# Performance work log

Measured on AMD Instinct MI355X. Metric: run time of the kernel, lower is better.

Reference implementation:

```python
import jax, jax.numpy as jnp
import numpy as np

KERNEL = 3  # unfold kernel size (stride 1, no padding)

def _unfold(x, k):
    # torch.nn.Unfold(kernel_size=k) equivalent: (B, C, H, W) -> (B, C*k*k, L)
    # channel ordering: index = c*k*k + i*k + j (channel outermost), matching torch.
    B, C, H, W = x.shape
    Ho, Wo = H - k + 1, W - k + 1
    cols = [x[:, :, i:i + Ho, j:j + Wo] for i in range(k) for j in range(k)]  # k*k x (B,C,Ho,Wo)
    u = jnp.stack(cols, axis=2)  # (B, C, k*k, Ho, Wo)
    return u.reshape(B, C * k * k, Ho * Wo)


def setup_inputs() -> dict:
    key = jax.random.key(0)
    k1, k2, k3, k4 = jax.random.split(key, 4)
    B, C, H, W = 512, 3, 64, 64
    M = 512            # num_neurons
    K = C * KERNEL * KERNEL   # input_dim = 27
    L = (H - KERNEL + 1) * (W - KERNEL + 1)  # 3844 patches
    O = 10             # output_dim
    x = jax.random.normal(k1, (B, C, H, W), dtype=jnp.float32)
    G = jax.random.normal(k2, (M, L), dtype=jnp.float32)
    # original inits v,w to zeros; use randn for a non-degenerate reference
    v = jax.random.normal(k3, (M, K, O), dtype=jnp.float32) * 0.02
    w = jax.random.normal(k4, (M, K, O), dtype=jnp.float32) * 0.02
    return {"x": x, "G": G, "v": v, "w": w}


def reference(x, G, v, w):
    # Faithful to:
    #   U = unfold(x)                         (B, K, L)
    #   t = einsum('mn,ikn->imnk', G, U)      (B, M, L, K)  <- never materialized here
    #   out = einsum('ijkl,jlm->im', t, v-w)  (B, O)
    # Reordered as two small contractions (same math, no huge intermediate):
    U = _unfold(x, KERNEL)                    # (B, K, L)
    A = jnp.einsum('bkn,mn->bmk', U, G)       # (B, M, K): contract over patches L
    p_diff = v - w                            # (M, K, O)
    out = jnp.einsum('bmk,mko->bo', A, p_diff)  # (B, O)
    return out
```

## Files before the change

### kernel.cpp

```cpp
#include <hip/hip_runtime.h>
#include <hip/hip_bf16.h>

#define ODIM   10
#define HOg    62
#define LDIM   3844
#define CHW    12288
#define BATCH  512
#define KO     270
#define KOP2   288
#define MDIM   512
#define NPAD   3968
#define LROW   72

typedef __attribute__((ext_vector_type(8))) short bfrag;
typedef __attribute__((ext_vector_type(4))) float f32x4;

__global__ __launch_bounds__(256)
void prep_kernel(const float* __restrict__ G,
                 const float* __restrict__ v, const float* __restrict__ w,
                 __hip_bfloat16* __restrict__ Gt,
                 __hip_bfloat16* __restrict__ Pdt,
                 float* __restrict__ out) {
    const int b = blockIdx.x;
    if (b < 496) {
        __shared__ float tile[64][65];
        const int nTile = b % 62;
        const int mTile = b / 62;
        const int n0 = nTile * 64;
        const int m0 = mTile * 64;
        const int tc = threadIdx.x & 63;
        const int tr = threadIdx.x >> 6;
#pragma unroll
        for (int rr = 0; rr < 64; rr += 4) {
            int n = n0 + tc;
            tile[rr + tr][tc] = (n < LDIM) ? G[(size_t)(m0 + rr + tr) * LDIM + n] : 0.f;
        }
        __syncthreads();
        const int nr = threadIdx.x >> 2;
        const int ms = (threadIdx.x & 3) * 16;
        __hip_bfloat16 buf[16];
#pragma unroll
        for (int i = 0; i < 16; ++i)
            buf[i] = __float2bfloat16(tile[ms + i][nr]);
        __hip_bfloat16* dst = Gt + (size_t)(n0 + nr) * MDIM + m0 + ms;
        *reinterpret_cast<uint4*>(dst)     = *reinterpret_cast<uint4*>(&buf[0]);
        *reinterpret_cast<uint4*>(dst + 8) = *reinterpret_cast<uint4*>(&buf[8]);
    } else if (b < 1072) {
        int idx = (b - 496) * 256 + threadIdx.x;
        int ko = idx >> 9;
        int m  = idx & 511;
        float val = (ko < KO) ? (v[m * KO + ko] - w[m * KO + ko]) : 0.f;
        Pdt[idx] = __float2bfloat16(val);
    } else {
        int idx = (b - 1072) * 256 + threadIdx.x;
        out[idx] = 0.f;
    }
}

__global__ __launch_bounds__(256, 2)
void tmfma_kernel(const __hip_bfloat16* __restrict__ Pdt,
                  const __hip_bfloat16* __restrict__ Gt,
                  float* __restrict__ T) {
    const int orig = blockIdx.x;
    const int xcd  = orig & 7;
    const int q8   = orig >> 3;
    const int lb   = (xcd < 7 ? xcd * 35 : 245) + (xcd < 7 ? q8 : q8);
    const int lbf  = (xcd < 7 ? xcd * 35 + q8 : 245 + q8);
    const int kt   = lbf % 9;
    const int nt   = lbf / 9;
    (void)lb;
    const int ko0  = kt * 32;
    const int n0   = nt * 128;

    const int tid  = threadIdx.x;
    const int wv   = tid >> 6;
    const int lane = tid & 63;
    const int r16  = lane & 15;
    const int kg   = lane >> 4;

    __shared__ __hip_bfloat16 ldsA[2][32 * LROW];
    __shared__ __hip_bfloat16 ldsB[2][128 * LROW];

    const int srow  = tid >> 3;
    const int slot  = tid & 7;
    const __hip_bfloat16* pA = Pdt + (size_t)(ko0 + srow) * MDIM + slot * 8;
    const __hip_bfloat16* pB0 = Gt + (size_t)(n0 +       srow) * MDIM + slot * 8;
    const __hip_bfloat16* pB1 = Gt + (size_t)(n0 +  32 + srow) * MDIM + slot * 8;
    const __hip_bfloat16* pB2 = Gt + (size_t)(n0 +  64 + srow) * MDIM + slot * 8;
    const __hip_bfloat16* pB3 = Gt + (size_t)(n0 +  96 + srow) * MDIM + slot * 8;
    const int aoff  = srow * LROW + slot * 8;
    const int boff0 = (      srow) * LROW + slot * 8;
    const int boff1 = ( 32 + srow) * LROW + slot * 8;
    const int boff2 = ( 64 + srow) * LROW + slot * 8;
    const int boff3 = ( 96 + srow) * LROW + slot * 8;

    f32x4 acc00 = {0.f,0.f,0.f,0.f}, acc01 = {0.f,0.f,0.f,0.f};
    f32x4 acc10 = {0.f,0.f,0.f,0.f}, acc11 = {0.f,0.f,0.f,0.f};

    uint4 rA, rB0, rB1, rB2, rB3;

#define LDREGS(t)                                                         \
    do { int k0 = (t) * 64;                                               \
        rA  = *reinterpret_cast<const uint4*>(pA  + k0);                  \
        rB0 = *reinterpret_cast<const uint4*>(pB0 + k0);                  \
        rB1 = *reinterpret_cast<const uint4*>(pB1 + k0);                  \
        rB2 = *reinterpret_cast<const uint4*>(pB2 + k0);                  \
        rB3 = *reinterpret_cast<const uint4*>(pB3 + k0);                  \
    } while (0)

#define WRLDS(bsel)                                                       \
    do {                                                                  \
        *reinterpret_cast<uint4*>(&ldsA[bsel][aoff])  = rA;               \
        *reinterpret_cast<uint4*>(&ldsB[bsel][boff0]) = rB0;              \
        *reinterpret_cast<uint4*>(&ldsB[bsel][boff1]) = rB1;              \
        *reinterpret_cast<uint4*>(&ldsB[bsel][boff2]) = rB2;              \
        *reinterpret_cast<uint4*>(&ldsB[bsel][boff3]) = rB3;              \
    } while (0)

#define COMPUTE(bsel)                                                     \
    do {                                                                  \
        _Pragma("unroll")                                                 \
        for (int ks = 0; ks < 2; ++ks) {                                  \
            int kb = ks * 32 + kg * 8;                                    \
            bfrag a0 = *reinterpret_cast<const bfrag*>(                   \
                &ldsA[bsel][(r16) * LROW + kb]);                          \
            bfrag a1 = *reinterpret_cast<const bfrag*>(                   \
                &ldsA[bsel][(16 + r16) * LROW + kb]);                     \
            bfrag b0 = *reinterpret_cast<const bfrag*>(                   \
                &ldsB[bsel][(wv * 32 + r16) * LROW + kb]);                \
            bfrag b1 = *reinterpret_cast<const bfrag*>(                   \
                &ldsB[bsel][(wv * 32 + 16 + r16) * LROW + kb]);           \
            acc00 = __builtin_amdgcn_mfma_f32_16x16x32_bf16(a0, b0, acc00, 0, 0, 0); \
            acc01 = __builtin_amdgcn_mfma_f32_16x16x32_bf16(a0, b1, acc01, 0, 0, 0); \
            acc10 = __builtin_amdgcn_mfma_f32_16x16x32_bf16(a1, b0, acc10, 0, 0, 0); \
            acc11 = __builtin_amdgcn_mfma_f32_16x16x32_bf16(a1, b1, acc11, 0, 0, 0); \
        }                                                                 \
    } while (0)

    LDREGS(0);
    WRLDS(0);
    __syncthreads();

#pragma unroll
    for (int t = 0; t < 8; ++t) {
        const int cur = t & 1;
        if (t < 7) LDREGS(t + 1);
        COMPUTE(cur);
        if (t < 7) WRLDS(cur ^ 1);
        __syncthreads();
    }
#undef LDREGS
#undef WRLDS
#undef COMPUTE

    const f32x4* accs[4] = { &acc00, &acc01, &acc10, &acc11 };
#pragma unroll
    for (int f = 0; f < 2; ++f) {
#pragma unroll
        for (int g = 0; g < 2; ++g) {
            const f32x4 a = *accs[f * 2 + g];
            int col = n0 + wv * 32 + g * 16 + r16;
            if (col < LDIM) {
#pragma unroll
                for (int r = 0; r < 4; ++r) {
                    int ro = ko0 + f * 16 + kg * 4 + r;
                    if (ro < KO)
                        T[(size_t)ro * LDIM + col] = a[r];
                }
            }
        }
    }
}

__global__ __launch_bounds__(256)
void fold_kernel(const float* __restrict__ T, float* __restrict__ S) {
    int idx = blockIdx.x * 256 + threadIdx.x;
    if (idx >= ODIM * CHW) return;
    int o   = idx / CHW;
    int chw = idx - o * CHW;
    int c = chw >> 12;
    int h = (chw >> 6) & 63;
    int w = chw & 63;

    float s = 0.f;
    for (int i = 0; i < 3; ++i) {
        int pi = h - i;
        if ((unsigned)pi >= HOg) continue;
        for (int j = 0; j < 3; ++j) {
            int pj = w - j;
            if ((unsigned)pj >= HOg) continue;
            int ko = (c * 9 + i * 3 + j) * ODIM + o;
            s += T[(size_t)ko * LDIM + pi * HOg + pj];
        }
    }
    S[idx] = s;
}

__global__ __launch_bounds__(256)
void out_gemm_kernel(const float* __restrict__ X,
                     const float* __restrict__ S,
                     float* __restrict__ out) {
    const int bg = blockIdx.x / 12;
    const int sl = blockIdx.x % 12;
    const int b0 = bg * 8;
    const int tid = threadIdx.x;
    const int NV = CHW / 4;
    const int i  = sl * 256 + tid;

    const float4* X4 = reinterpret_cast<const float4*>(X);
    const float4* S4 = reinterpret_cast<const float4*>(S);

    float acc[8][ODIM];
#pragma unroll
    for (int im = 0; im < 8; ++im)
#pragma unroll
        for (int o = 0; o < ODIM; ++o) acc[im][o] = 0.f;

    float4 xv[8];
#pragma unroll
    for (int im = 0; im < 8; ++im)
        xv[im] = X4[(size_t)(b0 + im) * NV + i];
#pragma unroll
    for (int o = 0; o < ODIM; ++o) {
        float4 sv = S4[(size_t)o * NV + i];
#pragma unroll
        for (int im = 0; im < 8; ++im) {
            acc[im][o] += xv[im].x * sv.x + xv[im].y * sv.y
                        + xv[im].z * sv.z + xv[im].w * sv.w;
        }
    }

#pragma unroll
    for (int im = 0; im < 8; ++im)
#pragma unroll
        for (int o = 0; o < ODIM; ++o) {
            float s = acc[im][o];
            for (int off = 32; off > 0; off >>= 1)
                s += __shfl_down(s, off, 64);
            acc[im][o] = s;
        }

    __shared__ float red[4][80];
    const int wave = tid >> 6;
    const int lane = tid & 63;
    if (lane == 0) {
#pragma unroll
        for (int im = 0; im < 8; ++im)
#pragma unroll
            for (int o = 0; o < ODIM; ++o)
                red[wave][im * ODIM + o] = acc[im][o];
    }
    __syncthreads();
    if (tid < 80) {
        float t = red[0][tid] + red[1][tid] + red[2][tid] + red[3][tid];
        int im = tid / ODIM;
        int o  = tid - im * ODIM;
        atomicAdd(&out[(size_t)(b0 + im) * ODIM + o], t);
    }
}

extern "C" void kernel_launch(void* const* d_in, const int* in_sizes, int n_in,
                              void* d_out, int out_size, void* d_ws, size_t ws_size,
                              hipStream_t stream) {
    const float* x = (const float*)d_in[0];
    const float* G = (const float*)d_in[1];
    const float* v = (const float*)d_in[2];
    const float* w = (const float*)d_in[3];
    float* out = (float*)d_out;

    char* wsb = (char*)d_ws;
    float*          T   = (float*)wsb;
    __hip_bfloat16* Gt  = (__hip_bfloat16*)(wsb + 4151520);
    __hip_bfloat16* Pdt = (__hip_bfloat16*)(wsb + 4151520 + 4063232);
    float*          S   = (float*)(wsb + 4151520 + 4063232 + 294912);

    prep_kernel<<<1092, 256, 0, stream>>>(G, v, w, Gt, Pdt, out);

    tmfma_kernel<<<279, 256, 0, stream>>>(Pdt, Gt, T);

    fold_kernel<<<(ODIM * CHW + 255) / 256, 256, 0, stream>>>(T, S);

    out_gemm_kernel<<<768, 256, 0, stream>>>(x, S, out);
}
```

Baseline: 45.38 us.

## Fuse fold into MFMA epilogue via atomics and split-K the GEMM in halves

The separate fold kernel and the intermediate T buffer are removed. The MFMA kernel now scatters each accumulator value directly into the folded S array with atomicAdd, and prep_kernel zeroes S beforehand. The GEMM also splits the M (reduction) dimension in two, which doubles the grid to 558 blocks with half the k-loop each, to fill more CUs. This saves one launch and the T write and re-read, but adds float atomic contention (up to 9 overlapping patch contributions per location plus 2 halves) and makes the summation order nondeterministic.

After: 49.11 us. +8.2%, slower.

```diff
diff --git a/kernel.cpp b/kernel.cpp
--- a/kernel.cpp
+++ b/kernel.cpp
@@ -7,9 +7,7 @@
 #define CHW    12288
 #define BATCH  512
 #define KO     270
-#define KOP2   288
 #define MDIM   512
-#define NPAD   3968
 #define LROW   72
 
 typedef __attribute__((ext_vector_type(8))) short bfrag;
@@ -20,6 +18,7 @@
                  const float* __restrict__ v, const float* __restrict__ w,
                  __hip_bfloat16* __restrict__ Gt,
                  __hip_bfloat16* __restrict__ Pdt,
+                 float* __restrict__ S,
                  float* __restrict__ out) {
     const int b = blockIdx.x;
     if (b < 496) {
@@ -51,8 +50,11 @@
         int m  = idx & 511;
         float val = (ko < KO) ? (v[m * KO + ko] - w[m * KO + ko]) : 0.f;
         Pdt[idx] = __float2bfloat16(val);
+    } else if (b < 1552) {
+        int idx = (b - 1072) * 256 + threadIdx.x;
+        S[idx] = 0.f;
     } else {
-        int idx = (b - 1072) * 256 + threadIdx.x;
+        int idx = (b - 1552) * 256 + threadIdx.x;
         out[idx] = 0.f;
     }
 }
@@ -60,17 +62,17 @@
 __global__ __launch_bounds__(256, 2)
 void tmfma_kernel(const __hip_bfloat16* __restrict__ Pdt,
                   const __hip_bfloat16* __restrict__ Gt,
-                  float* __restrict__ T) {
+                  float* __restrict__ S) {
     const int orig = blockIdx.x;
     const int xcd  = orig & 7;
     const int q8   = orig >> 3;
-    const int lb   = (xcd < 7 ? xcd * 35 : 245) + (xcd < 7 ? q8 : q8);
-    const int lbf  = (xcd < 7 ? xcd * 35 + q8 : 245 + q8);
-    const int kt   = lbf % 9;
-    const int nt   = lbf / 9;
-    (void)lb;
+    const int lb   = (xcd < 6 ? xcd * 70 : 420 + (xcd - 6) * 69) + q8;
+    const int half = lb & 1;
+    const int kt   = (lb >> 1) % 9;
+    const int nt   = (lb >> 1) / 9;
     const int ko0  = kt * 32;
     const int n0   = nt * 128;
+    const int mBase = half * 256;
 
     const int tid  = threadIdx.x;
     const int wv   = tid >> 6;
@@ -83,11 +85,11 @@
 
     const int srow  = tid >> 3;
     const int slot  = tid & 7;
-    const __hip_bfloat16* pA = Pdt + (size_t)(ko0 + srow) * MDIM + slot * 8;
-    const __hip_bfloat16* pB0 = Gt + (size_t)(n0 +       srow) * MDIM + slot * 8;
-    const __hip_bfloat16* pB1 = Gt + (size_t)(n0 +  32 + srow) * MDIM + slot * 8;
-    const __hip_bfloat16* pB2 = Gt + (size_t)(n0 +  64 + srow) * MDIM + slot * 8;
-    const __hip_bfloat16* pB3 = Gt + (size_t)(n0 +  96 + srow) * MDIM + slot * 8;
+    const __hip_bfloat16* pA  = Pdt + (size_t)(ko0 + srow) * MDIM + mBase + slot * 8;
+    const __hip_bfloat16* pB0 = Gt + (size_t)(n0 +       srow) * MDIM + mBase + slot * 8;
+    const __hip_bfloat16* pB1 = Gt + (size_t)(n0 +  32 + srow) * MDIM + mBase + slot * 8;
+    const __hip_bfloat16* pB2 = Gt + (size_t)(n0 +  64 + srow) * MDIM + mBase + slot * 8;
+    const __hip_bfloat16* pB3 = Gt + (size_t)(n0 +  96 + srow) * MDIM + mBase + slot * 8;
     const int aoff  = srow * LROW + slot * 8;
     const int boff0 = (      srow) * LROW + slot * 8;
     const int boff1 = ( 32 + srow) * LROW + slot * 8;
@@ -142,11 +144,11 @@
     __syncthreads();
 
 #pragma unroll
-    for (int t = 0; t < 8; ++t) {
+    for (int t = 0; t < 4; ++t) {
         const int cur = t & 1;
-        if (t < 7) LDREGS(t + 1);
+        if (t < 3) LDREGS(t + 1);
         COMPUTE(cur);
-        if (t < 7) WRLDS(cur ^ 1);
+        if (t < 3) WRLDS(cur ^ 1);
         __syncthreads();
     }
 #undef LDREGS
@@ -161,39 +163,25 @@
             const f32x4 a = *accs[f * 2 + g];
             int col = n0 + wv * 32 + g * 16 + r16;
             if (col < LDIM) {
+                int pi  = col / HOg;
+                int pj  = col - pi * HOg;
+                int off = pi * 64 + pj;
 #pragma unroll
                 for (int r = 0; r < 4; ++r) {
                     int ro = ko0 + f * 16 + kg * 4 + r;
-                    if (ro < KO)
-                        T[(size_t)ro * LDIM + col] = a[r];
+                    if (ro < KO) {
+                        int o   = ro % ODIM;
+                        int rem = ro / ODIM;
+                        int c   = rem / 9;
+                        int ij  = rem - c * 9;
+                        int i   = ij / 3;
+                        int jk  = ij - i * 3;
+                        atomicAdd(&S[o * CHW + c * 4096 + i * 64 + jk + off], a[r]);
+                    }
                 }
             }
         }
     }
-}
-
-__global__ __launch_bounds__(256)
-void fold_kernel(const float* __restrict__ T, float* __restrict__ S) {
-    int idx = blockIdx.x * 256 + threadIdx.x;
-    if (idx >= ODIM * CHW) return;
-    int o   = idx / CHW;
-    int chw = idx - o * CHW;
-    int c = chw >> 12;
-    int h = (chw >> 6) & 63;
-    int w = chw & 63;
-
-    float s = 0.f;
-    for (int i = 0; i < 3; ++i) {
-        int pi = h - i;
-        if ((unsigned)pi >= HOg) continue;
-        for (int j = 0; j < 3; ++j) {
-            int pj = w - j;
-            if ((unsigned)pj >= HOg) continue;
-            int ko = (c * 9 + i * 3 + j) * ODIM + o;
-            s += T[(size_t)ko * LDIM + pi * HOg + pj];
-        }
-    }
-    S[idx] = s;
 }
 
 __global__ __launch_bounds__(256)
@@ -269,16 +257,13 @@
     float* out = (float*)d_out;
 
     char* wsb = (char*)d_ws;
-    float*          T   = (float*)wsb;
-    __hip_bfloat16* Gt  = (__hip_bfloat16*)(wsb + 4151520);
-    __hip_bfloat16* Pdt = (__hip_bfloat16*)(wsb + 4151520 + 4063232);
-    float*          S   = (float*)(wsb + 4151520 + 4063232 + 294912);
-
-    prep_kernel<<<1092, 256, 0, stream>>>(G, v, w, Gt, Pdt, out);
-
-    tmfma_kernel<<<279, 256, 0, stream>>>(Pdt, Gt, T);
-
-    fold_kernel<<<(ODIM * CHW + 255) / 256, 256, 0, stream>>>(T, S);
+    float*          S   = (float*)wsb;
+    __hip_bfloat16* Gt  = (__hip_bfloat16*)(wsb + 491520);
+    __hip_bfloat16* Pdt = (__hip_bfloat16*)(wsb + 491520 + 4063232);
+
+    prep_kernel<<<1572, 256, 0, stream>>>(G, v, w, Gt, Pdt, S, out);
+
+    tmfma_kernel<<<558, 256, 0, stream>>>(Pdt, Gt, S);
 
     out_gemm_kernel<<<768, 256, 0, stream>>>(x, S, out);
 }
```
